# Optimization experiments

Hardware: AMD Instinct MI355X
Metric: run time of the kernel (lower is better)

The kernel has to match this reference:

```python
import jax, jax.numpy as jnp
import numpy as np

DEPTH = 2
DIM = 64
INNER = 256  # hard-coded inner_dim in Attention
HEADS = 1
N = 4096
B = 2
EPS = 1e-5


def layernorm(x, g, b):
    m = jnp.mean(x, axis=-1, keepdims=True)
    v = jnp.var(x, axis=-1, keepdims=True)
    return (x - m) * jax.lax.rsqrt(v + EPS) * g + b


def setup_inputs() -> dict:
    key = jax.random.key(0)
    ks = jax.random.split(key, 16)
    embed = jax.random.normal(ks[0], (B, N, DIM), dtype=jnp.float32)
    A = jax.random.randint(ks[1], (1, HEADS, N, N), 0, 2).astype(jnp.float32)
    s = 0.02
    return {
        "embed": embed,
        "A": A,
        "g1": jnp.ones((DEPTH, DIM), jnp.float32),
        "b1": jnp.zeros((DEPTH, DIM), jnp.float32),
        "Wqkv": jax.random.normal(ks[2], (DEPTH, DIM, INNER * 3), jnp.float32) * s,
        "Wout": jax.random.normal(ks[3], (DEPTH, INNER, DIM), jnp.float32) * s,
        "bout": jnp.zeros((DEPTH, DIM), jnp.float32),
        "g2": jnp.ones((DEPTH, DIM), jnp.float32),
        "b2": jnp.zeros((DEPTH, DIM), jnp.float32),
        "W1": jax.random.normal(ks[4], (DEPTH, DIM, DIM), jnp.float32) * s,
        "bb1": jnp.zeros((DEPTH, DIM), jnp.float32),
        "W2": jax.random.normal(ks[5], (DEPTH, DIM, DIM), jnp.float32) * s,
        "bb2": jnp.zeros((DEPTH, DIM), jnp.float32),
        "gf": jnp.ones((DIM,), jnp.float32),
        "bf": jnp.zeros((DIM,), jnp.float32),
    }


def _encoder(embed, A, g1, b1, Wqkv, Wout, bout, g2, b2, W1, bb1, W2, bb2, gf, bf):
    b, n, dim = embed.shape
    scale = dim ** (-0.5)
    dh = INNER // HEADS
    x = embed
    attn = None
    dots_softmax = None
    diag = jnp.arange(n)
    for l in range(DEPTH):
        xn = layernorm(x, g1[l], b1[l])
        qkv = xn @ Wqkv[l]  # [b, n, 3*INNER]
        q, k, v = jnp.split(qkv, 3, axis=-1)
        # [b, n, INNER] -> [b, h, n, dh]
        q = q.reshape(b, n, HEADS, dh).transpose(0, 2, 1, 3)
        k = k.reshape(b, n, HEADS, dh).transpose(0, 2, 1, 3)
        v = v.reshape(b, n, HEADS, dh).transpose(0, 2, 1, 3)
        dots = jnp.einsum("bhid,bhjd->bhij", q, k) * scale
        dots_softmax = jax.nn.softmax(dots[0, 0], axis=-1)
        # adjacency mask, then only [0][0] kept; diagonal filled with literal 1.0;
        # the original does a cpu/numpy roundtrip with .detach() -> stop_gradient.
        e = jnp.where(A > 0, dots, jnp.float32(-9e15))[0, 0]  # [n, n]
        e = e.at[diag, diag].set(1.0)
        e = jax.lax.stop_gradient(e)
        attn = jax.nn.softmax(e, axis=-1)  # [n, n], shared across b, h
        out = jnp.einsum("ij,bhjd->bhid", attn, v)  # broadcast attn over b,h
        out = out.transpose(0, 2, 1, 3).reshape(b, n, INNER)
        out = out @ Wout[l] + bout[l]
        x = xn + out  # residual onto the NORMED input (as in original)
        xm = layernorm(x, g2[l], b2[l])
        mlp = jax.nn.gelu(xm @ W1[l] + bb1[l], approximate=False) @ W2[l] + bb2[l]
        x = xm + mlp
    x = layernorm(x, gf, bf)
    return x, attn.reshape(1, 1, n, n), dots_softmax


def reference(embed, A, g1, b1, Wqkv, Wout, bout, g2, b2, W1, bb1, W2, bb2, gf, bf):
    return _encoder(embed, A, g1, b1, Wqkv, Wout, bout, g2, b2, W1, bb1, W2, bb2, gf, bf)
```

## Files before the change

kernel.cpp:

```cpp
#include <hip/hip_runtime.h>
#include <hip/hip_bf16.h>
#include <math.h>

typedef __attribute__((ext_vector_type(8))) short short8;
typedef __attribute__((ext_vector_type(4))) float f32x4;

#define NG 16

__device__ __forceinline__ unsigned short f2bf(float x) {
    __hip_bfloat16 b = __float2bfloat16(x);
    return *reinterpret_cast<unsigned short*>(&b);
}
__device__ __forceinline__ float bf2f(unsigned short u) {
    unsigned int t = ((unsigned int)u) << 16;
    float f;
    __builtin_memcpy(&f, &t, 4);
    return f;
}
__device__ __forceinline__ float gelu_exact(float x) {
    return 0.5f * x * (1.0f + erff(x * 0.70710678118654752f));
}

__global__ __launch_bounds__(256) void k_zero(float* __restrict__ p, long n)
{
    long i = (long)blockIdx.x * 256 + threadIdx.x;
    if (i < n) p[i] = 0.f;
}

__global__ __launch_bounds__(256) void k_layernorm(
    const float* __restrict__ x, const float* __restrict__ g,
    const float* __restrict__ b, float* __restrict__ out)
{
    int wave = threadIdx.x >> 6, lane = threadIdx.x & 63;
    long row = (long)blockIdx.x * 4 + wave;
    float v = x[row * 64 + lane];
    float s = v;
    #pragma unroll
    for (int o = 32; o; o >>= 1) s += __shfl_xor(s, o);
    float m = s * (1.0f / 64.0f);
    float d = v - m;
    float q = d * d;
    #pragma unroll
    for (int o = 32; o; o >>= 1) q += __shfl_xor(q, o);
    float rstd = rsqrtf(q * (1.0f / 64.0f) + 1e-5f);
    out[row * 64 + lane] = d * rstd * g[lane] + b[lane];
}

__global__ __launch_bounds__(256) void k_wfold(
    const float* __restrict__ Wqkv, const float* __restrict__ Wout,
    float* __restrict__ Wfold)
{
    int l = blockIdx.x >> 4;
    int idx = (blockIdx.x & 15) * 256 + threadIdx.x;
    int c = idx >> 6, d = idx & 63;
    const float* Wq = Wqkv + (long)l * 64 * 768;
    const float* Wo = Wout + (long)l * 256 * 64;
    float a = 0.f;
    for (int k = 0; k < 256; ++k)
        a += Wq[c * 768 + 512 + k] * Wo[k * 64 + d];
    Wfold[l * 4096 + idx] = a;
}

__global__ __launch_bounds__(256) void k_maskpack(
    const float* __restrict__ Aadj, unsigned long long* __restrict__ mask)
{
    int row = blockIdx.x;
    int wave = threadIdx.x >> 6, lane = threadIdx.x & 63;
    for (int w = wave; w < 64; w += 4) {
        float a = Aadj[(long)row * 4096 + w * 64 + lane];
        unsigned long long m = __ballot(a > 0.f);
        if (lane == 0) mask[(long)row * 64 + w] = m;
    }
}

__global__ __launch_bounds__(256) void k_qk(
    const float* __restrict__ xn, const float* __restrict__ W,
    unsigned short* __restrict__ q, unsigned short* __restrict__ kmat)
{
    __shared__ float As[64][65];
    __shared__ float Ws[64][65];
    int tid = threadIdx.x;
    int m0 = blockIdx.x * 64, n0 = blockIdx.y * 64;
    #pragma unroll
    for (int it = 0; it < 16; ++it) {
        int idx = tid + it * 256;
        int r = idx >> 6, c = idx & 63;
        As[r][c] = xn[(long)(m0 + r) * 64 + c];
        Ws[r][c] = W[(long)r * 768 + n0 + c];
    }
    __syncthreads();
    int tx = tid & 15, ty = tid >> 4;
    float acc[4][4] = {};
    #pragma unroll
    for (int k = 0; k < 64; ++k) {
        float a[4], w[4];
        #pragma unroll
        for (int i = 0; i < 4; ++i) a[i] = As[ty * 4 + i][k];
        #pragma unroll
        for (int j = 0; j < 4; ++j) w[j] = Ws[k][tx * 4 + j];
        #pragma unroll
        for (int i = 0; i < 4; ++i)
            #pragma unroll
            for (int j = 0; j < 4; ++j) acc[i][j] += a[i] * w[j];
    }
    #pragma unroll
    for (int i = 0; i < 4; ++i) {
        long row = m0 + ty * 4 + i;
        #pragma unroll
        for (int j = 0; j < 4; ++j) {
            int col = n0 + tx * 4 + j;
            if (col < 256) q[row * 256 + col] = f2bf(acc[i][j]);
            else           kmat[row * 256 + (col - 256)] = f2bf(acc[i][j]);
        }
    }
}

__global__ __launch_bounds__(256) void k_xnw_t(
    const float* __restrict__ xn, const float* __restrict__ Wfold,
    unsigned short* __restrict__ vWT)
{
    __shared__ float As[64][65];
    __shared__ float Ws[64][65];
    int tid = threadIdx.x;
    int n0 = blockIdx.x * 64, b = blockIdx.y;
    #pragma unroll
    for (int it = 0; it < 16; ++it) {
        int idx = tid + it * 256;
        int r = idx >> 6, c = idx & 63;
        As[r][c] = xn[((long)b * 4096 + n0 + r) * 64 + c];
        Ws[r][c] = Wfold[r * 64 + c];
    }
    __syncthreads();
    int tx = tid & 15, ty = tid >> 4;
    float acc[4][4] = {};
    #pragma unroll
    for (int k = 0; k < 64; ++k) {
        float a[4], w[4];
        #pragma unroll
        for (int i = 0; i < 4; ++i) a[i] = As[ty * 4 + i][k];
        #pragma unroll
        for (int j = 0; j < 4; ++j) w[j] = Ws[k][tx * 4 + j];
        #pragma unroll
        for (int i = 0; i < 4; ++i)
            #pragma unroll
            for (int j = 0; j < 4; ++j) acc[i][j] += a[i] * w[j];
    }
    #pragma unroll
    for (int i = 0; i < 4; ++i)
        #pragma unroll
        for (int j = 0; j < 4; ++j)
            vWT[((long)b * 64 + tx * 4 + j) * 4096 + n0 + ty * 4 + i] = f2bf(acc[i][j]);
}

__global__ __launch_bounds__(256) void k_flash(
    const unsigned short* __restrict__ q, const unsigned short* __restrict__ kmat,
    const unsigned short* __restrict__ vwt,
    const unsigned long long* __restrict__ mask, const float* __restrict__ Aadj,
    unsigned short* __restrict__ part,
    float* __restrict__ stats)
{
    __shared__ __align__(16) unsigned short Qs[128 * 64];
    __shared__ __align__(16) unsigned short Ks[128 * 64];
    __shared__ __align__(16) unsigned short Ps[128 * 128];
    int tid = threadIdx.x;
    int lane = tid & 63, wq = tid >> 6;
    int fr = lane & 15, quad = lane >> 4;
    int m0 = blockIdx.x * 128;
    int g  = blockIdx.y;

    f32x4 accO[2][8];
    #pragma unroll
    for (int i = 0; i < 2; ++i)
        #pragma unroll
        for (int j = 0; j < 8; ++j) accO[i][j] = (f32x4){0.f, 0.f, 0.f, 0.f};
    float m_run[2] = {-1e30f, -1e30f};
    float s_run[2] = {0.f, 0.f};

    for (int jt = 0; jt < 2; ++jt) {
        int jb = g * 256 + jt * 128;
        f32x4 accS[8][2];
        #pragma unroll
        for (int i = 0; i < 8; ++i)
            #pragma unroll
            for (int n = 0; n < 2; ++n) accS[i][n] = (f32x4){0.f, 0.f, 0.f, 0.f};
        for (int k0 = 0; k0 < 256; k0 += 64) {
            #pragma unroll
            for (int it = 0; it < 4; ++it) {
                int idx = tid + it * 256;
                int r = idx >> 3, c8 = (idx & 7) * 8;
                *(short8*)&Qs[idx * 8] = *(const short8*)(q    + (long)(m0 + r) * 256 + k0 + c8);
                *(short8*)&Ks[idx * 8] = *(const short8*)(kmat + (long)(jb + r) * 256 + k0 + c8);
            }
            __syncthreads();
            #pragma unroll
            for (int ks = 0; ks < 2; ++ks) {
                short8 ka[8], qb[2];
                #pragma unroll
                for (int i = 0; i < 8; ++i)
                    ka[i] = *(const short8*)&Ks[(i * 16 + fr) * 64 + ks * 32 + quad * 8];
                #pragma unroll
                for (int n = 0; n < 2; ++n)
                    qb[n] = *(const short8*)&Qs[(wq * 32 + n * 16 + fr) * 64 + ks * 32 + quad * 8];
                #pragma unroll
                for (int i = 0; i < 8; ++i)
                    #pragma unroll
                    for (int n = 0; n < 2; ++n)
                        accS[i][n] = __builtin_amdgcn_mfma_f32_16x16x32_bf16(
                            ka[i], qb[n], accS[i][n], 0, 0, 0);
            }
            __syncthreads();
        }
        float al[2];
        #pragma unroll
        for (int n = 0; n < 2; ++n) {
            int qrow = m0 + wq * 32 + n * 16 + fr;
            unsigned long long mw0 = 0, mw1 = 0;
            if (mask) {
                mw0 = mask[(long)qrow * 64 + (jb >> 6)];
                mw1 = mask[(long)qrow * 64 + (jb >> 6) + 1];
            }
            float tm = -1e30f;
            #pragma unroll
            for (int i = 0; i < 8; ++i) {
                #pragma unroll
                for (int r = 0; r < 4; ++r) {
                    int jl = i * 16 + quad * 4 + r;
                    float v = accS[i][n][r] * 0.125f;
                    bool keep = mask ? (((jl < 64 ? (mw0 >> jl) : (mw1 >> (jl - 64))) & 1ull) != 0)
                                     : (Aadj[(long)qrow * 4096 + jb + jl] > 0.f);
                    v = keep ? v : -1e30f;
                    if (jb + jl == qrow) v = 1.0f;
                    accS[i][n][r] = v;
                    tm = fmaxf(tm, v);
                }
            }
            tm = fmaxf(tm, __shfl_xor(tm, 16));
            tm = fmaxf(tm, __shfl_xor(tm, 32));
            float mnew = fmaxf(fmaxf(m_run[n], tm), -1e20f);
            al[n] = __expf(m_run[n] - mnew);
            m_run[n] = mnew;
            float ts = 0.f;
            int qrl = wq * 32 + n * 16 + fr;
            #pragma unroll
            for (int i = 0; i < 8; ++i) {
                float p0 = __expf(accS[i][n][0] - mnew);
                float p1 = __expf(accS[i][n][1] - mnew);
                float p2 = __expf(accS[i][n][2] - mnew);
                float p3 = __expf(accS[i][n][3] - mnew);
                ts += (p0 + p1) + (p2 + p3);
                unsigned int lo = (unsigned int)f2bf(p0) | ((unsigned int)f2bf(p1) << 16);
                unsigned int hi = (unsigned int)f2bf(p2) | ((unsigned int)f2bf(p3) << 16);
                int u = (qrl * 128 + i * 16 + quad * 4) ^ ((fr & 7) << 3);
                *(uint2*)&Ps[u] = make_uint2(lo, hi);
            }
            ts += __shfl_xor(ts, 16);
            ts += __shfl_xor(ts, 32);
            s_run[n] = s_run[n] * al[n] + ts;
        }
        #pragma unroll
        for (int ii = 0; ii < 2; ++ii) {
            float av[4];
            #pragma unroll
            for (int r = 0; r < 4; ++r) av[r] = __shfl(al[ii], quad * 4 + r);
            #pragma unroll
            for (int nn = 0; nn < 8; ++nn)
                #pragma unroll
                for (int r = 0; r < 4; ++r) accO[ii][nn][r] *= av[r];
        }
        #pragma unroll
        for (int it = 0; it < 4; ++it) {
            int idx = tid + it * 256;
            int r = idx >> 3, c8 = (idx & 7) * 8;
            *(short8*)&Qs[idx * 8] = *(const short8*)(vwt + (long)r * 4096 + jb + c8);
            *(short8*)&Ks[idx * 8] = *(const short8*)(vwt + (long)r * 4096 + jb + 64 + c8);
        }
        __syncthreads();
        #pragma unroll
        for (int ks4 = 0; ks4 < 4; ++ks4) {
            const unsigned short* buf = (ks4 < 2) ? Qs : Ks;
            int ksl = ks4 & 1;
            short8 pa[2], vb[8];
            #pragma unroll
            for (int ii = 0; ii < 2; ++ii) {
                int u = ((wq * 32 + ii * 16 + fr) * 128 + ks4 * 32 + quad * 8) ^ ((fr & 7) << 3);
                pa[ii] = *(const short8*)&Ps[u];
            }
            #pragma unroll
            for (int nn = 0; nn < 8; ++nn)
                vb[nn] = *(const short8*)&buf[(nn * 16 + fr) * 64 + ksl * 32 + quad * 8];
            #pragma unroll
            for (int ii = 0; ii < 2; ++ii)
                #pragma unroll
                for (int nn = 0; nn < 8; ++nn)
                    accO[ii][nn] = __builtin_amdgcn_mfma_f32_16x16x32_bf16(
                        pa[ii], vb[nn], accO[ii][nn], 0, 0, 0);
        }
        __syncthreads();
    }
    #pragma unroll
    for (int ii = 0; ii < 2; ++ii) {
        #pragma unroll
        for (int nn = 0; nn < 8; ++nn) {
            int ch = nn * 16 + fr;
            long rowb = m0 + wq * 32 + ii * 16 + quad * 4;
            #pragma unroll
            for (int r = 0; r < 4; ++r)
                part[((long)g * 4096 + rowb + r) * 128 + ch] = f2bf(accO[ii][nn][r]);
        }
    }
    if (quad == 0) {
        #pragma unroll
        for (int n = 0; n < 2; ++n) {
            int qrow = m0 + wq * 32 + n * 16 + fr;
            stats[((long)g * 4096 + qrow) * 2]     = m_run[n];
            stats[((long)g * 4096 + qrow) * 2 + 1] = s_run[n];
        }
    }
}

__global__ __launch_bounds__(256) void k_mfma_nt(
    const unsigned short* __restrict__ A, const unsigned short* __restrict__ B,
    float* __restrict__ C, int N, int K, float scale)
{
    __shared__ __align__(16) unsigned short As[128 * 64];
    __shared__ __align__(16) unsigned short Bs[128 * 64];
    int tid = threadIdx.x;
    int lane = tid & 63, wave = tid >> 6;
    long m0 = (long)blockIdx.x * 128, n0 = (long)blockIdx.y * 128;
    const unsigned short* Ag = A + m0 * K;
    const unsigned short* Bg = B + n0 * K;
    int wm = (wave & 1) * 64, wn = (wave >> 1) * 64;
    int fr = lane & 15, quad = lane >> 4;

    f32x4 acc[4][4];
    #pragma unroll
    for (int i = 0; i < 4; ++i)
        #pragma unroll
        for (int j = 0; j < 4; ++j) acc[i][j] = (f32x4){0.f, 0.f, 0.f, 0.f};

    for (int k0 = 0; k0 < K; k0 += 64) {
        #pragma unroll
        for (int it = 0; it < 4; ++it) {
            int c = tid + it * 256;
            int r = c >> 3, col = (c & 7) * 8;
            *(short8*)&As[c * 8] = *(const short8*)(Ag + (long)r * K + k0 + col);
            *(short8*)&Bs[c * 8] = *(const short8*)(Bg + (long)r * K + k0 + col);
        }
        __syncthreads();
        #pragma unroll
        for (int ks = 0; ks < 2; ++ks) {
            short8 af[4], bfr[4];
            #pragma unroll
            for (int i = 0; i < 4; ++i) {
                af[i]  = *(const short8*)&As[(wm + i * 16 + fr) * 64 + ks * 32 + quad * 8];
                bfr[i] = *(const short8*)&Bs[(wn + i * 16 + fr) * 64 + ks * 32 + quad * 8];
            }
            #pragma unroll
            for (int i = 0; i < 4; ++i)
                #pragma unroll
                for (int j = 0; j < 4; ++j)
                    acc[i][j] = __builtin_amdgcn_mfma_f32_16x16x32_bf16(
                        af[i], bfr[j], acc[i][j], 0, 0, 0);
        }
        __syncthreads();
    }
    #pragma unroll
    for (int i = 0; i < 4; ++i) {
        #pragma unroll
        for (int j = 0; j < 4; ++j) {
            long col = n0 + wn + j * 16 + fr;
            long rowb = m0 + wm + i * 16 + quad * 4;
            #pragma unroll
            for (int r = 0; r < 4; ++r)
                C[(rowb + r) * N + col] = acc[i][j][r] * scale;
        }
    }
}

__global__ __launch_bounds__(256) void k_mfma_splitk(
    const float* __restrict__ A, const unsigned short* __restrict__ B,
    float* __restrict__ C)
{
    __shared__ __align__(16) unsigned short As[128 * 64];
    __shared__ __align__(16) unsigned short Bs[128 * 64];
    const int K = 4096, N = 128;
    int tid = threadIdx.x;
    int lane = tid & 63, wave = tid >> 6;
    long m0 = (long)blockIdx.x * 128;
    int k0base = blockIdx.y * 512;
    const float* Ag = A + m0 * K;
    int wm = (wave & 1) * 64, wn = (wave >> 1) * 64;
    int fr = lane & 15, quad = lane >> 4;

    f32x4 acc[4][4];
    #pragma unroll
    for (int i = 0; i < 4; ++i)
        #pragma unroll
        for (int j = 0; j < 4; ++j) acc[i][j] = (f32x4){0.f, 0.f, 0.f, 0.f};

    for (int k0 = k0base; k0 < k0base + 512; k0 += 64) {
        #pragma unroll
        for (int it = 0; it < 4; ++it) {
            int c = tid + it * 256;
            int r = c >> 3, col = (c & 7) * 8;
            float4 f0 = *(const float4*)(Ag + (long)r * K + k0 + col);
            float4 f1 = *(const float4*)(Ag + (long)r * K + k0 + col + 4);
            short8 s;
            s[0] = (short)f2bf(f0.x); s[1] = (short)f2bf(f0.y);
            s[2] = (short)f2bf(f0.z); s[3] = (short)f2bf(f0.w);
            s[4] = (short)f2bf(f1.x); s[5] = (short)f2bf(f1.y);
            s[6] = (short)f2bf(f1.z); s[7] = (short)f2bf(f1.w);
            *(short8*)&As[c * 8] = s;
            *(short8*)&Bs[c * 8] = *(const short8*)(B + (long)r * K + k0 + col);
        }
        __syncthreads();
        #pragma unroll
        for (int ks = 0; ks < 2; ++ks) {
            short8 af[4], bfr[4];
            #pragma unroll
            for (int i = 0; i < 4; ++i) {
                af[i]  = *(const short8*)&As[(wm + i * 16 + fr) * 64 + ks * 32 + quad * 8];
                bfr[i] = *(const short8*)&Bs[(wn + i * 16 + fr) * 64 + ks * 32 + quad * 8];
            }
            #pragma unroll
            for (int i = 0; i < 4; ++i)
                #pragma unroll
                for (int j = 0; j < 4; ++j)
                    acc[i][j] = __builtin_amdgcn_mfma_f32_16x16x32_bf16(
                        af[i], bfr[j], acc[i][j], 0, 0, 0);
        }
        __syncthreads();
    }
    #pragma unroll
    for (int i = 0; i < 4; ++i) {
        #pragma unroll
        for (int j = 0; j < 4; ++j) {
            long col = wn + j * 16 + fr;
            long rowb = m0 + wm + i * 16 + quad * 4;
            #pragma unroll
            for (int r = 0; r < 4; ++r)
                atomicAdd(&C[(rowb + r) * N + col], acc[i][j][r]);
        }
    }
}

__device__ __forceinline__ float block_max(float v, float* red, int lane, int wave) {
    #pragma unroll
    for (int o = 32; o; o >>= 1) v = fmaxf(v, __shfl_xor(v, o));
    if (lane == 0) red[wave] = v;
    __syncthreads();
    v = fmaxf(fmaxf(red[0], red[1]), fmaxf(red[2], red[3]));
    __syncthreads();
    return v;
}
__device__ __forceinline__ float block_sum(float v, float* red, int lane, int wave) {
    #pragma unroll
    for (int o = 32; o; o >>= 1) v += __shfl_xor(v, o);
    if (lane == 0) red[wave] = v;
    __syncthreads();
    v = red[0] + red[1] + red[2] + red[3];
    __syncthreads();
    return v;
}

__global__ __launch_bounds__(256) void k_softmax_attn(
    float* __restrict__ dots, const float* __restrict__ Aadj,
    const unsigned long long* __restrict__ mask,
    float* __restrict__ attn_out, int write_ds)
{
    __shared__ float red[4];
    __shared__ unsigned long long msk[64];
    int row = blockIdx.x, tid = threadIdx.x;
    int lane = tid & 63, wave = tid >> 6;
    float* drow = dots + (long)row * 4096;
    if (mask) {
        if (tid < 64) msk[tid] = mask[(long)row * 64 + tid];
        __syncthreads();
    }
    float d[16], mv[16];
    float mmax = -1e30f, umax = -1e30f;
    #pragma unroll
    for (int i = 0; i < 16; ++i) {
        int j = tid + i * 256;
        float dv = drow[j];
        d[i] = dv;
        bool keep = mask ? ((msk[j >> 6] >> (j & 63)) & 1ull)
                         : (Aadj[(long)row * 4096 + j] > 0.f);
        float m = keep ? dv : -1e30f;
        if (j == row) m = 1.0f;
        mv[i] = m;
        mmax = fmaxf(mmax, m);
        umax = fmaxf(umax, dv);
    }
    float M1 = block_max(mmax, red, lane, wave);
    float s1 = 0.f;
    #pragma unroll
    for (int i = 0; i < 16; ++i) { float e = expf(mv[i] - M1); mv[i] = e; s1 += e; }
    s1 = block_sum(s1, red, lane, wave);
    float inv1 = 1.0f / s1;
    #pragma unroll
    for (int i = 0; i < 16; ++i)
        attn_out[(long)row * 4096 + tid + i * 256] = mv[i] * inv1;

    if (write_ds) {
        float M2 = block_max(umax, red, lane, wave);
        float s2 = 0.f;
        #pragma unroll
        for (int i = 0; i < 16; ++i) { float e = expf(d[i] - M2); d[i] = e; s2 += e; }
        s2 = block_sum(s2, red, lane, wave);
        float inv2 = 1.0f / s2;
        #pragma unroll
        for (int i = 0; i < 16; ++i)
            drow[tid + i * 256] = d[i] * inv2;
    }
}

__global__ __launch_bounds__(256) void k_avres_ln(
    const float* __restrict__ xn, const float* __restrict__ avcat,
    const float* __restrict__ bout, const float* __restrict__ g,
    const float* __restrict__ b, float* __restrict__ out)
{
    int wave = threadIdx.x >> 6, lane = threadIdx.x & 63;
    long row = (long)blockIdx.x * 4 + wave;
    int bb = (int)(row >> 12), n = (int)(row & 4095);
    float v = xn[row * 64 + lane] + avcat[(long)n * 128 + bb * 64 + lane] + bout[lane];
    float s = v;
    #pragma unroll
    for (int o = 32; o; o >>= 1) s += __shfl_xor(s, o);
    float m = s * (1.0f / 64.0f);
    float d = v - m;
    float q = d * d;
    #pragma unroll
    for (int o = 32; o; o >>= 1) q += __shfl_xor(q, o);
    float rstd = rsqrtf(q * (1.0f / 64.0f) + 1e-5f);
    out[row * 64 + lane] = d * rstd * g[lane] + b[lane];
}

__global__ __launch_bounds__(256) void k_avres_ln_c(
    const float* __restrict__ xn, const unsigned short* __restrict__ part,
    const float* __restrict__ stats, const float* __restrict__ bout,
    const float* __restrict__ g, const float* __restrict__ b,
    float* __restrict__ out)
{
    int wave = threadIdx.x >> 6, lane = threadIdx.x & 63;
    long row = (long)blockIdx.x * 4 + wave;
    int bb = (int)(row >> 12), n = (int)(row & 4095);
    float sm[NG], ss[NG];
    float ms = -1e30f;
    #pragma unroll
    for (int gg = 0; gg < NG; ++gg) {
        sm[gg] = stats[((long)gg * 4096 + n) * 2];
        ss[gg] = stats[((long)gg * 4096 + n) * 2 + 1];
        ms = fmaxf(ms, sm[gg]);
    }
    float acc = 0.f, stot = 0.f;
    #pragma unroll
    for (int gg = 0; gg < NG; ++gg) {
        float w = __expf(sm[gg] - ms);
        stot += w * ss[gg];
        acc  += w * bf2f(part[((long)gg * 4096 + n) * 128 + bb * 64 + lane]);
    }
    float v = xn[row * 64 + lane] + acc / stot + bout[lane];
    float s = v;
    #pragma unroll
    for (int o = 32; o; o >>= 1) s += __shfl_xor(s, o);
    float m = s * (1.0f / 64.0f);
    float d = v - m;
    float qv = d * d;
    #pragma unroll
    for (int o = 32; o; o >>= 1) qv += __shfl_xor(qv, o);
    float rstd = rsqrtf(qv * (1.0f / 64.0f) + 1e-5f);
    out[row * 64 + lane] = d * rstd * g[lane] + b[lane];
}

__global__ __launch_bounds__(256) void k_mlp(
    const float* __restrict__ xm,
    const float* __restrict__ W1, const float* __restrict__ bb1,
    const float* __restrict__ W2, const float* __restrict__ bb2,
    const float* __restrict__ g, const float* __restrict__ b,
    float* __restrict__ out)
{
    __shared__ float As[64][65];
    __shared__ float W1s[64][65];
    __shared__ float W2s[64][65];
    int tid = threadIdx.x;
    int m0 = blockIdx.x * 64;
    #pragma unroll
    for (int it = 0; it < 16; ++it) {
        int idx = tid + it * 256;
        int r = idx >> 6, c = idx & 63;
        As[r][c]  = xm[(long)(m0 + r) * 64 + c];
        W1s[r][c] = W1[(long)r * 64 + c];
        W2s[r][c] = W2[(long)r * 64 + c];
    }
    __syncthreads();
    int tx = tid & 15, ty = tid >> 4;
    float acc[4][4] = {};
    #pragma unroll
    for (int k = 0; k < 64; ++k) {
        float a[4], w[4];
        #pragma unroll
        for (int i = 0; i < 4; ++i) a[i] = As[ty * 4 + i][k];
        #pragma unroll
        for (int j = 0; j < 4; ++j) w[j] = W1s[k][tx * 4 + j];
        #pragma unroll
        for (int i = 0; i < 4; ++i)
            #pragma unroll
            for (int j = 0; j < 4; ++j) acc[i][j] += a[i] * w[j];
    }
    __syncthreads();
    #pragma unroll
    for (int i = 0; i < 4; ++i)
        #pragma unroll
        for (int j = 0; j < 4; ++j)
            W1s[ty * 4 + i][tx * 4 + j] = gelu_exact(acc[i][j] + bb1[tx * 4 + j]);
    __syncthreads();
    float acc2[4][4] = {};
    #pragma unroll
    for (int k = 0; k < 64; ++k) {
        float a[4], w[4];
        #pragma unroll
        for (int i = 0; i < 4; ++i) a[i] = W1s[ty * 4 + i][k];
        #pragma unroll
        for (int j = 0; j < 4; ++j) w[j] = W2s[k][tx * 4 + j];
        #pragma unroll
        for (int i = 0; i < 4; ++i)
            #pragma unroll
            for (int j = 0; j < 4; ++j) acc2[i][j] += a[i] * w[j];
    }
    #pragma unroll
    for (int i = 0; i < 4; ++i) {
        float v[4];
        float s = 0.f;
        #pragma unroll
        for (int j = 0; j < 4; ++j) {
            v[j] = acc2[i][j] + bb2[tx * 4 + j] + As[ty * 4 + i][tx * 4 + j];
            s += v[j];
        }
        #pragma unroll
        for (int o = 1; o < 16; o <<= 1) s += __shfl_xor(s, o);
        float m = s * (1.0f / 64.0f);
        float q = 0.f;
        #pragma unroll
        for (int j = 0; j < 4; ++j) { float d = v[j] - m; q += d * d; }
        #pragma unroll
        for (int o = 1; o < 16; o <<= 1) q += __shfl_xor(q, o);
        float rstd = rsqrtf(q * (1.0f / 64.0f) + 1e-5f);
        long row = m0 + ty * 4 + i;
        #pragma unroll
        for (int j = 0; j < 4; ++j) {
            int col = tx * 4 + j;
            out[row * 64 + col] = (v[j] - m) * rstd * g[col] + b[col];
        }
    }
}

extern "C" void kernel_launch(void* const* d_in, const int* in_sizes, int n_in,
                              void* d_out, int out_size, void* d_ws, size_t ws_size,
                              hipStream_t stream)
{
    const float* embed = (const float*)d_in[0];
    const float* Aadj  = (const float*)d_in[1];
    const float* g1    = (const float*)d_in[2];
    const float* b1    = (const float*)d_in[3];
    const float* Wqkv  = (const float*)d_in[4];
    const float* Wout  = (const float*)d_in[5];
    const float* bout  = (const float*)d_in[6];
    const float* g2    = (const float*)d_in[7];
    const float* b2    = (const float*)d_in[8];
    const float* W1    = (const float*)d_in[9];
    const float* bb1   = (const float*)d_in[10];
    const float* W2    = (const float*)d_in[11];
    const float* bb2   = (const float*)d_in[12];
    const float* gf    = (const float*)d_in[13];
    const float* bff   = (const float*)d_in[14];

    float* ox    = (float*)d_out;
    float* attnb = ox + 524288;
    float* dsb   = attnb + 16777216;

    if (ws_size < (10ull << 20)) {
        k_zero<<<133120, 256, 0, stream>>>(ox, 34078720l);
        return;
    }

    char* ws = (char*)d_ws;
    float*          xn    = (float*)(ws + (2l << 20));
    unsigned short* q     = (unsigned short*)(ws + (6l << 20));
    unsigned short* kmat  = (unsigned short*)(ws + (7l << 20));
    unsigned short* vwt   = (unsigned short*)(ws + (8l << 20));
    float*          Wfold = (float*)(ws + (9l << 20));
    unsigned long long* mask = (ws_size >= (12ull << 20))
        ? (unsigned long long*)(ws + (10l << 20)) : nullptr;

    unsigned short* part   = (unsigned short*)attnb;
    float*          fstats = attnb + 4194304;

    if (mask) k_maskpack<<<4096, 256, 0, stream>>>(Aadj, mask);
    k_wfold<<<32, 256, 0, stream>>>(Wqkv, Wout, Wfold);

    k_layernorm<<<2048, 256, 0, stream>>>(embed, g1, b1, xn);
    k_qk<<<dim3(64, 8), 256, 0, stream>>>(xn, Wqkv, q, kmat);
    k_xnw_t<<<dim3(64, 2), 256, 0, stream>>>(xn, Wfold, vwt);
    k_flash<<<dim3(32, NG), 256, 0, stream>>>(q, kmat, vwt, mask, Aadj, part, fstats);
    k_avres_ln_c<<<2048, 256, 0, stream>>>(xn, part, fstats, bout, g2, b2, xn);
    k_mlp<<<128, 256, 0, stream>>>(xn, W1, bb1, W2, bb2,
                                   g1 + 64, b1 + 64, xn);

    k_qk<<<dim3(64, 8), 256, 0, stream>>>(xn, Wqkv + 64 * 768, q, kmat);
    k_xnw_t<<<dim3(64, 2), 256, 0, stream>>>(xn, Wfold + 4096, vwt);
    k_mfma_nt<<<dim3(32, 32), 256, 0, stream>>>(q, kmat, dsb, 4096, 256, 0.125f);
    k_softmax_attn<<<4096, 256, 0, stream>>>(dsb, Aadj, mask, attnb, 1);
    k_zero<<<2048, 256, 0, stream>>>(ox, 524288l);
    k_mfma_splitk<<<dim3(32, 8), 256, 0, stream>>>(attnb, vwt, ox);
    k_avres_ln<<<2048, 256, 0, stream>>>(xn, ox, bout + 64, g2 + 64, b2 + 64, xn);
    k_mlp<<<128, 256, 0, stream>>>(xn, W1 + 4096, bb1 + 64, W2 + 4096, bb2 + 64,
                                   gf, bff, ox);
}
```

Measured before the change: 463.9 us.

## Fuse prologue kernels, store layer-2 dots as bf16, vectorize softmax I/O

Merges mask packing, weight folding, the first layernorm and zeroing of the split-K accumulator into one prologue launch, and merges the q/k projection with the folded-V projection into one launch. Layer-2 dots are now written as bf16 into the attention output region instead of fp32 into the dots-softmax buffer. A new softmax kernel reads the bf16 row and writes both the masked attention and the unmasked softmax with float4 stores. The aim is fewer launches and less HBM traffic on the 4096x4096 matrices, at the cost of bf16 rounding of the dots before the softmax and some branch divergence inside the fused kernels.

```diff
diff --git a/kernel.cpp b/kernel.cpp
--- a/kernel.cpp
+++ b/kernel.cpp
@@ -27,129 +27,128 @@
     if (i < n) p[i] = 0.f;
 }
 
-__global__ __launch_bounds__(256) void k_layernorm(
-    const float* __restrict__ x, const float* __restrict__ g,
-    const float* __restrict__ b, float* __restrict__ out)
-{
-    int wave = threadIdx.x >> 6, lane = threadIdx.x & 63;
-    long row = (long)blockIdx.x * 4 + wave;
-    float v = x[row * 64 + lane];
-    float s = v;
-    #pragma unroll
-    for (int o = 32; o; o >>= 1) s += __shfl_xor(s, o);
-    float m = s * (1.0f / 64.0f);
-    float d = v - m;
-    float q = d * d;
-    #pragma unroll
-    for (int o = 32; o; o >>= 1) q += __shfl_xor(q, o);
-    float rstd = rsqrtf(q * (1.0f / 64.0f) + 1e-5f);
-    out[row * 64 + lane] = d * rstd * g[lane] + b[lane];
-}
-
-__global__ __launch_bounds__(256) void k_wfold(
+__global__ __launch_bounds__(256) void k_prologue(
+    const float* __restrict__ Aadj, unsigned long long* __restrict__ mask,
     const float* __restrict__ Wqkv, const float* __restrict__ Wout,
-    float* __restrict__ Wfold)
-{
-    int l = blockIdx.x >> 4;
-    int idx = (blockIdx.x & 15) * 256 + threadIdx.x;
-    int c = idx >> 6, d = idx & 63;
-    const float* Wq = Wqkv + (long)l * 64 * 768;
-    const float* Wo = Wout + (long)l * 256 * 64;
-    float a = 0.f;
-    for (int k = 0; k < 256; ++k)
-        a += Wq[c * 768 + 512 + k] * Wo[k * 64 + d];
-    Wfold[l * 4096 + idx] = a;
-}
-
-__global__ __launch_bounds__(256) void k_maskpack(
-    const float* __restrict__ Aadj, unsigned long long* __restrict__ mask)
-{
-    int row = blockIdx.x;
-    int wave = threadIdx.x >> 6, lane = threadIdx.x & 63;
-    for (int w = wave; w < 64; w += 4) {
-        float a = Aadj[(long)row * 4096 + w * 64 + lane];
-        unsigned long long m = __ballot(a > 0.f);
-        if (lane == 0) mask[(long)row * 64 + w] = m;
-    }
-}
-
-__global__ __launch_bounds__(256) void k_qk(
+    float* __restrict__ Wfold,
+    const float* __restrict__ embed, const float* __restrict__ g1,
+    const float* __restrict__ b1, float* __restrict__ xn,
+    float* __restrict__ zbuf)
+{
+    int bx = blockIdx.x, tid = threadIdx.x;
+    if (bx < 4096) {
+        if (!mask) return;
+        int row = bx;
+        int wave = tid >> 6, lane = tid & 63;
+        for (int w = wave; w < 64; w += 4) {
+            float a = Aadj[(long)row * 4096 + w * 64 + lane];
+            unsigned long long m = __ballot(a > 0.f);
+            if (lane == 0) mask[(long)row * 64 + w] = m;
+        }
+    } else if (bx < 4128) {
+        int bid = bx - 4096;
+        int l = bid >> 4;
+        int idx = (bid & 15) * 256 + tid;
+        int c = idx >> 6, d = idx & 63;
+        const float* Wq = Wqkv + (long)l * 64 * 768;
+        const float* Wo = Wout + (long)l * 256 * 64;
+        float a = 0.f;
+        for (int k = 0; k < 256; ++k)
+            a += Wq[c * 768 + 512 + k] * Wo[k * 64 + d];
+        Wfold[l * 4096 + idx] = a;
+    } else if (bx < 6176) {
+        int wave = tid >> 6, lane = tid & 63;
+        long row = (long)(bx - 4128) * 4 + wave;
+        float v = embed[row * 64 + lane];
+        float s = v;
+        #pragma unroll
+        for (int o = 32; o; o >>= 1) s += __shfl_xor(s, o);
+        float m = s * (1.0f / 64.0f);
+        float d = v - m;
+        float q = d * d;
+        #pragma unroll
+        for (int o = 32; o; o >>= 1) q += __shfl_xor(q, o);
+        float rstd = rsqrtf(q * (1.0f / 64.0f) + 1e-5f);
+        xn[row * 64 + lane] = d * rstd * g1[lane] + b1[lane];
+    } else {
+        long i = (long)(bx - 6176) * 256 + tid;
+        if (i < 524288) zbuf[i] = 0.f;
+    }
+}
+
+__global__ __launch_bounds__(256) void k_qkx(
     const float* __restrict__ xn, const float* __restrict__ W,
-    unsigned short* __restrict__ q, unsigned short* __restrict__ kmat)
+    const float* __restrict__ Wfold,
+    unsigned short* __restrict__ q, unsigned short* __restrict__ kmat,
+    unsigned short* __restrict__ vWT)
 {
     __shared__ float As[64][65];
     __shared__ float Ws[64][65];
     int tid = threadIdx.x;
-    int m0 = blockIdx.x * 64, n0 = blockIdx.y * 64;
-    #pragma unroll
-    for (int it = 0; it < 16; ++it) {
-        int idx = tid + it * 256;
-        int r = idx >> 6, c = idx & 63;
-        As[r][c] = xn[(long)(m0 + r) * 64 + c];
-        Ws[r][c] = W[(long)r * 768 + n0 + c];
-    }
-    __syncthreads();
+    int by = blockIdx.y;
     int tx = tid & 15, ty = tid >> 4;
-    float acc[4][4] = {};
-    #pragma unroll
-    for (int k = 0; k < 64; ++k) {
-        float a[4], w[4];
-        #pragma unroll
-        for (int i = 0; i < 4; ++i) a[i] = As[ty * 4 + i][k];
-        #pragma unroll
-        for (int j = 0; j < 4; ++j) w[j] = Ws[k][tx * 4 + j];
+    if (by < 8) {
+        int m0 = blockIdx.x * 64, n0 = by * 64;
+        #pragma unroll
+        for (int it = 0; it < 16; ++it) {
+            int idx = tid + it * 256;
+            int r = idx >> 6, c = idx & 63;
+            As[r][c] = xn[(long)(m0 + r) * 64 + c];
+            Ws[r][c] = W[(long)r * 768 + n0 + c];
+        }
+        __syncthreads();
+        float acc[4][4] = {};
+        #pragma unroll
+        for (int k = 0; k < 64; ++k) {
+            float a[4], w[4];
+            #pragma unroll
+            for (int i = 0; i < 4; ++i) a[i] = As[ty * 4 + i][k];
+            #pragma unroll
+            for (int j = 0; j < 4; ++j) w[j] = Ws[k][tx * 4 + j];
+            #pragma unroll
+            for (int i = 0; i < 4; ++i)
+                #pragma unroll
+                for (int j = 0; j < 4; ++j) acc[i][j] += a[i] * w[j];
+        }
+        #pragma unroll
+        for (int i = 0; i < 4; ++i) {
+            long row = m0 + ty * 4 + i;
+            #pragma unroll
+            for (int j = 0; j < 4; ++j) {
+                int col = n0 + tx * 4 + j;
+                if (col < 256) q[row * 256 + col] = f2bf(acc[i][j]);
+                else           kmat[row * 256 + (col - 256)] = f2bf(acc[i][j]);
+            }
+        }
+    } else {
+        int n0 = blockIdx.x * 64, b = by - 8;
+        #pragma unroll
+        for (int it = 0; it < 16; ++it) {
+            int idx = tid + it * 256;
+            int r = idx >> 6, c = idx & 63;
+            As[r][c] = xn[((long)b * 4096 + n0 + r) * 64 + c];
+            Ws[r][c] = Wfold[r * 64 + c];
+        }
+        __syncthreads();
+        float acc[4][4] = {};
+        #pragma unroll
+        for (int k = 0; k < 64; ++k) {
+            float a[4], w[4];
+            #pragma unroll
+            for (int i = 0; i < 4; ++i) a[i] = As[ty * 4 + i][k];
+            #pragma unroll
+            for (int j = 0; j < 4; ++j) w[j] = Ws[k][tx * 4 + j];
+            #pragma unroll
+            for (int i = 0; i < 4; ++i)
+                #pragma unroll
+                for (int j = 0; j < 4; ++j) acc[i][j] += a[i] * w[j];
+        }
         #pragma unroll
         for (int i = 0; i < 4; ++i)
             #pragma unroll
-            for (int j = 0; j < 4; ++j) acc[i][j] += a[i] * w[j];
-    }
-    #pragma unroll
-    for (int i = 0; i < 4; ++i) {
-        long row = m0 + ty * 4 + i;
-        #pragma unroll
-        for (int j = 0; j < 4; ++j) {
-            int col = n0 + tx * 4 + j;
-            if (col < 256) q[row * 256 + col] = f2bf(acc[i][j]);
-            else           kmat[row * 256 + (col - 256)] = f2bf(acc[i][j]);
-        }
-    }
-}
-
-__global__ __launch_bounds__(256) void k_xnw_t(
-    const float* __restrict__ xn, const float* __restrict__ Wfold,
-    unsigned short* __restrict__ vWT)
-{
-    __shared__ float As[64][65];
-    __shared__ float Ws[64][65];
-    int tid = threadIdx.x;
-    int n0 = blockIdx.x * 64, b = blockIdx.y;
-    #pragma unroll
-    for (int it = 0; it < 16; ++it) {
-        int idx = tid + it * 256;
-        int r = idx >> 6, c = idx & 63;
-        As[r][c] = xn[((long)b * 4096 + n0 + r) * 64 + c];
-        Ws[r][c] = Wfold[r * 64 + c];
-    }
-    __syncthreads();
-    int tx = tid & 15, ty = tid >> 4;
-    float acc[4][4] = {};
-    #pragma unroll
-    for (int k = 0; k < 64; ++k) {
-        float a[4], w[4];
-        #pragma unroll
-        for (int i = 0; i < 4; ++i) a[i] = As[ty * 4 + i][k];
-        #pragma unroll
-        for (int j = 0; j < 4; ++j) w[j] = Ws[k][tx * 4 + j];
-        #pragma unroll
-        for (int i = 0; i < 4; ++i)
-            #pragma unroll
-            for (int j = 0; j < 4; ++j) acc[i][j] += a[i] * w[j];
-    }
-    #pragma unroll
-    for (int i = 0; i < 4; ++i)
-        #pragma unroll
-        for (int j = 0; j < 4; ++j)
-            vWT[((long)b * 64 + tx * 4 + j) * 4096 + n0 + ty * 4 + i] = f2bf(acc[i][j]);
+            for (int j = 0; j < 4; ++j)
+                vWT[((long)b * 64 + tx * 4 + j) * 4096 + n0 + ty * 4 + i] = f2bf(acc[i][j]);
+    }
 }
 
 __global__ __launch_bounds__(256) void k_flash(
@@ -320,7 +319,7 @@
 
 __global__ __launch_bounds__(256) void k_mfma_nt(
     const unsigned short* __restrict__ A, const unsigned short* __restrict__ B,
-    float* __restrict__ C, int N, int K, float scale)
+    unsigned short* __restrict__ Cb, int ld, int K, float scale)
 {
     __shared__ __align__(16) unsigned short As[128 * 64];
     __shared__ __align__(16) unsigned short Bs[128 * 64];
@@ -372,9 +371,92 @@
             long rowb = m0 + wm + i * 16 + quad * 4;
             #pragma unroll
             for (int r = 0; r < 4; ++r)
-                C[(rowb + r) * N + col] = acc[i][j][r] * scale;
-        }
-    }
+                Cb[(rowb + r) * ld + col] = f2bf(acc[i][j][r] * scale);
+        }
+    }
+}
+
+__device__ __forceinline__ float block_max(float v, float* red, int lane, int wave) {
+    #pragma unroll
+    for (int o = 32; o; o >>= 1) v = fmaxf(v, __shfl_xor(v, o));
+    if (lane == 0) red[wave] = v;
+    __syncthreads();
+    v = fmaxf(fmaxf(red[0], red[1]), fmaxf(red[2], red[3]));
+    __syncthreads();
+    return v;
+}
+__device__ __forceinline__ float block_sum(float v, float* red, int lane, int wave) {
+    #pragma unroll
+    for (int o = 32; o; o >>= 1) v += __shfl_xor(v, o);
+    if (lane == 0) red[wave] = v;
+    __syncthreads();
+    v = red[0] + red[1] + red[2] + red[3];
+    __syncthreads();
+    return v;
+}
+
+__global__ __launch_bounds__(256) void k_softmax_io(
+    const unsigned short* __restrict__ dots_b, const float* __restrict__ Aadj,
+    const unsigned long long* __restrict__ mask,
+    float* __restrict__ attn, float* __restrict__ ds)
+{
+    __shared__ float red[4];
+    __shared__ unsigned long long msk[64];
+    int row = blockIdx.x, tid = threadIdx.x;
+    int lane = tid & 63, wave = tid >> 6;
+    if (mask) {
+        if (tid < 64) msk[tid] = mask[(long)row * 64 + tid];
+        __syncthreads();
+    }
+    const unsigned short* drow = dots_b + (long)row * 8192 + tid * 16;
+    short8 dv0 = *(const short8*)drow;
+    short8 dv1 = *(const short8*)(drow + 8);
+    unsigned long long mword = mask ? msk[tid >> 2] : 0ull;
+    int bitbase = (tid & 3) * 16;
+    float d[16], mv[16];
+    float mmax = -1e30f, umax = -1e30f;
+    #pragma unroll
+    for (int i = 0; i < 16; ++i) {
+        unsigned short u = (unsigned short)(i < 8 ? dv0[i] : dv1[i - 8]);
+        float dvf = bf2f(u);
+        int j = tid * 16 + i;
+        d[i] = dvf;
+        bool keep = mask ? ((mword >> (bitbase + i)) & 1ull)
+                         : (Aadj[(long)row * 4096 + j] > 0.f);
+        float m = keep ? dvf : -1e30f;
+        if (j == row) m = 1.0f;
+        mv[i] = m;
+        mmax = fmaxf(mmax, m);
+        umax = fmaxf(umax, dvf);
+    }
+    float M1 = block_max(mmax, red, lane, wave);
+    float s1 = 0.f;
+    #pragma unroll
+    for (int i = 0; i < 16; ++i) { float e = expf(mv[i] - M1); mv[i] = e; s1 += e; }
+    s1 = block_sum(s1, red, lane, wave);
+    float inv1 = 1.0f / s1;
+    float4 o0, o1, o2, o3;
+    o0 = make_float4(mv[0] * inv1, mv[1] * inv1, mv[2] * inv1, mv[3] * inv1);
+    o1 = make_float4(mv[4] * inv1, mv[5] * inv1, mv[6] * inv1, mv[7] * inv1);
+    o2 = make_float4(mv[8] * inv1, mv[9] * inv1, mv[10] * inv1, mv[11] * inv1);
+    o3 = make_float4(mv[12] * inv1, mv[13] * inv1, mv[14] * inv1, mv[15] * inv1);
+    float* arow = attn + (long)row * 4096 + tid * 16;
+    *(float4*)(arow + 0)  = o0;
+    *(float4*)(arow + 4)  = o1;
+    *(float4*)(arow + 8)  = o2;
+    *(float4*)(arow + 12) = o3;
+
+    float M2 = block_max(umax, red, lane, wave);
+    float s2 = 0.f;
+    #pragma unroll
+    for (int i = 0; i < 16; ++i) { float e = expf(d[i] - M2); d[i] = e; s2 += e; }
+    s2 = block_sum(s2, red, lane, wave);
+    float inv2 = 1.0f / s2;
+    float* srow = ds + (long)row * 4096 + tid * 16;
+    *(float4*)(srow + 0)  = make_float4(d[0] * inv2, d[1] * inv2, d[2] * inv2, d[3] * inv2);
+    *(float4*)(srow + 4)  = make_float4(d[4] * inv2, d[5] * inv2, d[6] * inv2, d[7] * inv2);
+    *(float4*)(srow + 8)  = make_float4(d[8] * inv2, d[9] * inv2, d[10] * inv2, d[11] * inv2);
+    *(float4*)(srow + 12) = make_float4(d[12] * inv2, d[13] * inv2, d[14] * inv2, d[15] * inv2);
 }
 
 __global__ __launch_bounds__(256) void k_mfma_splitk(
@@ -441,77 +523,6 @@
             for (int r = 0; r < 4; ++r)
                 atomicAdd(&C[(rowb + r) * N + col], acc[i][j][r]);
         }
-    }
-}
-
-__device__ __forceinline__ float block_max(float v, float* red, int lane, int wave) {
-    #pragma unroll
-    for (int o = 32; o; o >>= 1) v = fmaxf(v, __shfl_xor(v, o));
-    if (lane == 0) red[wave] = v;
-    __syncthreads();
-    v = fmaxf(fmaxf(red[0], red[1]), fmaxf(red[2], red[3]));
-    __syncthreads();
-    return v;
-}
-__device__ __forceinline__ float block_sum(float v, float* red, int lane, int wave) {
-    #pragma unroll
-    for (int o = 32; o; o >>= 1) v += __shfl_xor(v, o);
-    if (lane == 0) red[wave] = v;
-    __syncthreads();
-    v = red[0] + red[1] + red[2] + red[3];
-    __syncthreads();
-    return v;
-}
-
-__global__ __launch_bounds__(256) void k_softmax_attn(
-    float* __restrict__ dots, const float* __restrict__ Aadj,
-    const unsigned long long* __restrict__ mask,
-    float* __restrict__ attn_out, int write_ds)
-{
-    __shared__ float red[4];
-    __shared__ unsigned long long msk[64];
-    int row = blockIdx.x, tid = threadIdx.x;
-    int lane = tid & 63, wave = tid >> 6;
-    float* drow = dots + (long)row * 4096;
-    if (mask) {
-        if (tid < 64) msk[tid] = mask[(long)row * 64 + tid];
-        __syncthreads();
-    }
-    float d[16], mv[16];
-    float mmax = -1e30f, umax = -1e30f;
-    #pragma unroll
-    for (int i = 0; i < 16; ++i) {
-        int j = tid + i * 256;
-        float dv = drow[j];
-        d[i] = dv;
-        bool keep = mask ? ((msk[j >> 6] >> (j & 63)) & 1ull)
-                         : (Aadj[(long)row * 4096 + j] > 0.f);
-        float m = keep ? dv : -1e30f;
-        if (j == row) m = 1.0f;
-        mv[i] = m;
-        mmax = fmaxf(mmax, m);
-        umax = fmaxf(umax, dv);
-    }
-    float M1 = block_max(mmax, red, lane, wave);
-    float s1 = 0.f;
-    #pragma unroll
-    for (int i = 0; i < 16; ++i) { float e = expf(mv[i] - M1); mv[i] = e; s1 += e; }
-    s1 = block_sum(s1, red, lane, wave);
-    float inv1 = 1.0f / s1;
-    #pragma unroll
-    for (int i = 0; i < 16; ++i)
-        attn_out[(long)row * 4096 + tid + i * 256] = mv[i] * inv1;
-
-    if (write_ds) {
-        float M2 = block_max(umax, red, lane, wave);
-        float s2 = 0.f;
-        #pragma unroll
-        for (int i = 0; i < 16; ++i) { float e = expf(d[i] - M2); d[i] = e; s2 += e; }
-        s2 = block_sum(s2, red, lane, wave);
-        float inv2 = 1.0f / s2;
-        #pragma unroll
-        for (int i = 0; i < 16; ++i)
-            drow[tid + i * 256] = d[i] * inv2;
     }
 }
 
@@ -685,35 +696,33 @@
     }
 
     char* ws = (char*)d_ws;
-    float*          xn    = (float*)(ws + (2l << 20));
-    unsigned short* q     = (unsigned short*)(ws + (6l << 20));
-    unsigned short* kmat  = (unsigned short*)(ws + (7l << 20));
-    unsigned short* vwt   = (unsigned short*)(ws + (8l << 20));
-    float*          Wfold = (float*)(ws + (9l << 20));
+    float*          avcat  = (float*)(ws + (0l << 20));
+    float*          xn     = (float*)(ws + (2l << 20));
+    unsigned short* q      = (unsigned short*)(ws + (6l << 20));
+    unsigned short* kmat   = (unsigned short*)(ws + (7l << 20));
+    unsigned short* vwt    = (unsigned short*)(ws + (8l << 20));
+    float*          Wfold  = (float*)(ws + (9l << 20));
     unsigned long long* mask = (ws_size >= (12ull << 20))
         ? (unsigned long long*)(ws + (10l << 20)) : nullptr;
 
     unsigned short* part   = (unsigned short*)attnb;
     float*          fstats = attnb + 4194304;
-
-    if (mask) k_maskpack<<<4096, 256, 0, stream>>>(Aadj, mask);
-    k_wfold<<<32, 256, 0, stream>>>(Wqkv, Wout, Wfold);
-
-    k_layernorm<<<2048, 256, 0, stream>>>(embed, g1, b1, xn);
-    k_qk<<<dim3(64, 8), 256, 0, stream>>>(xn, Wqkv, q, kmat);
-    k_xnw_t<<<dim3(64, 2), 256, 0, stream>>>(xn, Wfold, vwt);
+    unsigned short* dots_b = (unsigned short*)attnb;
+
+    k_prologue<<<8224, 256, 0, stream>>>(Aadj, mask, Wqkv, Wout, Wfold,
+                                         embed, g1, b1, xn, avcat);
+
+    k_qkx<<<dim3(64, 10), 256, 0, stream>>>(xn, Wqkv, Wfold, q, kmat, vwt);
     k_flash<<<dim3(32, NG), 256, 0, stream>>>(q, kmat, vwt, mask, Aadj, part, fstats);
     k_avres_ln_c<<<2048, 256, 0, stream>>>(xn, part, fstats, bout, g2, b2, xn);
     k_mlp<<<128, 256, 0, stream>>>(xn, W1, bb1, W2, bb2,
                                    g1 + 64, b1 + 64, xn);
 
-    k_qk<<<dim3(64, 8), 256, 0, stream>>>(xn, Wqkv + 64 * 768, q, kmat);
-    k_xnw_t<<<dim3(64, 2), 256, 0, stream>>>(xn, Wfold + 4096, vwt);
-    k_mfma_nt<<<dim3(32, 32), 256, 0, stream>>>(q, kmat, dsb, 4096, 256, 0.125f);
-    k_softmax_attn<<<4096, 256, 0, stream>>>(dsb, Aadj, mask, attnb, 1);
-    k_zero<<<2048, 256, 0, stream>>>(ox, 524288l);
-    k_mfma_splitk<<<dim3(32, 8), 256, 0, stream>>>(attnb, vwt, ox);
-    k_avres_ln<<<2048, 256, 0, stream>>>(xn, ox, bout + 64, g2 + 64, b2 + 64, xn);
+    k_qkx<<<dim3(64, 10), 256, 0, stream>>>(xn, Wqkv + 64 * 768, Wfold + 4096, q, kmat, vwt);
+    k_mfma_nt<<<dim3(32, 32), 256, 0, stream>>>(q, kmat, dots_b, 8192, 256, 0.125f);
+    k_softmax_io<<<4096, 256, 0, stream>>>(dots_b, Aadj, mask, attnb, dsb);
+    k_mfma_splitk<<<dim3(32, 8), 256, 0, stream>>>(attnb, vwt, avcat);
+    k_avres_ln<<<2048, 256, 0, stream>>>(xn, avcat, bout + 64, g2 + 64, b2 + 64, xn);
     k_mlp<<<128, 256, 0, stream>>>(xn, W1 + 4096, bb1 + 64, W2 + 4096, bb2 + 64,
                                    gf, bff, ox);
 }
```

New measurement: 464.5 us. About the same (+0.1%).
